# Kernel optimization log

Measured on AMD Instinct MI355X. Metric: run time of the kernel, lower is better.

The kernel has to match this reference:

```python
import jax, jax.numpy as jnp
import numpy as np

N = 50000
E = 800000
D_IN, D_HID, D_OUT = 128, 128, 64


def setup_inputs() -> dict:
    key = jax.random.key(0)
    ks = jax.random.split(key, 8)
    x = jax.random.normal(ks[0], (N, D_IN), dtype=jnp.float32)
    edge_index = jax.random.randint(ks[1], (2, E), 0, N, dtype=jnp.int64)
    # Glorot-ish init for GCNConv linear weights + zero bias (PyG default bias=True)
    def lin(k, din, dout):
        s = 1.0 / np.sqrt(din)
        return jax.random.uniform(k, (din, dout), jnp.float32, -s, s)
    return {
        "x": x,
        "edge_index": edge_index,
        "W1": lin(ks[2], D_IN, D_HID), "b1": jnp.zeros((D_HID,), jnp.float32),
        "W2": lin(ks[3], D_HID, D_HID), "b2": jnp.zeros((D_HID,), jnp.float32),
        "W3": lin(ks[4], D_HID, D_OUT), "b3": jnp.zeros((D_OUT,), jnp.float32),
    }


def _prep_edges(edge_index, n):
    # add self loops (PyG GCNConv default add_self_loops=True)
    loop = jnp.arange(n, dtype=edge_index.dtype)
    src = jnp.concatenate([edge_index[0], loop])
    dst = jnp.concatenate([edge_index[1], loop])
    deg = jax.ops.segment_sum(jnp.ones_like(dst, dtype=jnp.float32), dst, num_segments=n)
    dinv = jnp.where(deg > 0, jax.lax.rsqrt(deg), 0.0)
    norm = dinv[src] * dinv[dst]  # symmetric normalization per edge
    return src, dst, norm


def _gcn_conv(h, W, b, src, dst, norm, n):
    h = h @ W                                   # [N, dout]
    msg = h[src] * norm[:, None]                # [E+N, dout] gather
    out = jax.ops.segment_sum(msg, dst, num_segments=n)  # scatter-add
    return out + b


def reference(x, edge_index, W1, b1, W2, b2, W3, b3):
    src, dst, norm = _prep_edges(edge_index, N)
    h = jax.nn.relu(_gcn_conv(x, W1, b1, src, dst, norm, N))
    h = jax.nn.relu(_gcn_conv(h, W2, b2, src, dst, norm, N))
    return _gcn_conv(h, W3, b3, src, dst, norm, N)  # eval mode: dropout is identity
```

## Files before the change

kernel.cpp:

```cpp
#include <hip/hip_runtime.h>
#include <hip/hip_fp16.h>
#include <math.h>

#define NN 50000
#define NE 800000
#define RSTRIDE 104
#define RAWSTRIDE 96
#define NBUCK 196
#define BCAP 4608
#define ACH 4096

using bf8v = __attribute__((ext_vector_type(8))) short;
using f4v  = __attribute__((ext_vector_type(4))) float;

__device__ inline unsigned short f2bf(float f) {
    unsigned int u = __float_as_uint(f);
    u += 0x7FFFu + ((u >> 16) & 1u);
    return (unsigned short)(u >> 16);
}
__device__ inline float bflo(unsigned int d) { return __uint_as_float(d << 16); }
__device__ inline float bfhi(unsigned int d) { return __uint_as_float(d & 0xFFFF0000u); }
__device__ inline float ew(unsigned int u) {
    return __half2float(__ushort_as_half((unsigned short)(u >> 16)));
}
__device__ inline unsigned int epack(int col, float w) {
    return (unsigned int)col | ((unsigned int)__half_as_ushort(__float2half(w)) << 16);
}


__global__ __launch_bounds__(256) void bin_kernel(const int* __restrict__ src,
                                                  const int* __restrict__ dst,
                                                  int* __restrict__ gcursor,
                                                  unsigned int* __restrict__ bst) {
    __shared__ unsigned int items[ACH];
    __shared__ int cnt[256], pref[257], gstart[256];
    const int t = threadIdx.x;
    cnt[t] = 0;
    __syncthreads();
    const int base = blockIdx.x * ACH;

    unsigned int my[16]; int myb[16], myr[16];
    #pragma unroll
    for (int i = 0; i < 16; ++i) {
        int e = base + i * 256 + t;
        my[i] = 0; myb[i] = -1; myr[i] = 0;
        if (e < NE) {
            int d = dst[e], s = src[e];
            my[i] = (unsigned int)s | ((unsigned int)d << 16);
            int b = d >> 8;
            myb[i] = b;
            myr[i] = atomicAdd(&cnt[b], 1);
        }
    }
    __syncthreads();
    if (t == 0) {
        int run = 0;
        for (int b = 0; b < 256; ++b) { pref[b] = run; run += cnt[b]; }
        pref[256] = run;
    }
    __syncthreads();
    if (cnt[t] > 0) gstart[t] = atomicAdd(&gcursor[t], cnt[t]);
    __syncthreads();
    #pragma unroll
    for (int i = 0; i < 16; ++i)
        if (myb[i] >= 0) items[pref[myb[i]] + myr[i]] = my[i];
    __syncthreads();
    const int total = pref[256];
    for (int i = t; i < total; i += 256) {
        int lo = 0, hi = 255;
        while (lo < hi) { int mid = (lo + hi + 1) >> 1; if (pref[mid] <= i) lo = mid; else hi = mid - 1; }
        int idx = gstart[lo] + (i - pref[lo]);
        if (idx < BCAP) bst[(size_t)lo * BCAP + idx] = items[i];
    }
}


__global__ __launch_bounds__(512) void sortb_kernel(const int* __restrict__ gcursor,
                                                    const unsigned int* __restrict__ bst,
                                                    int* __restrict__ cnt_g,
                                                    float* __restrict__ dinv,
                                                    unsigned short* __restrict__ raw) {
    __shared__ unsigned int items[BCAP];
    __shared__ int cnt[256], pref[257], cur[256];
    __shared__ unsigned short outl[BCAP];
    const int b = blockIdx.x;
    const int t = threadIdx.x;
    int n = gcursor[b];
    if (n > BCAP) n = BCAP;
    if (t < 256) { cnt[t] = 0; cur[t] = 0; }
    __syncthreads();
    for (int i = t; i < n; i += 512) {
        unsigned int u = bst[(size_t)b * BCAP + i];
        items[i] = u;
        atomicAdd(&cnt[(u >> 16) & 255], 1);
    }
    __syncthreads();
    if (t == 0) {
        int run = 0;
        for (int j = 0; j < 256; ++j) { pref[j] = run; run += cnt[j]; }
        pref[256] = run;
    }
    __syncthreads();
    for (int i = t; i < n; i += 512) {
        unsigned int u = items[i];
        int ln = (u >> 16) & 255;
        int r = atomicAdd(&cur[ln], 1);
        outl[pref[ln] + r] = (unsigned short)(u & 0xFFFFu);
    }
    __syncthreads();
    for (int i = t; i < n; i += 512) {
        int lo = 0, hi = 255;
        while (lo < hi) { int mid = (lo + hi + 1) >> 1; if (pref[mid] <= i) lo = mid; else hi = mid - 1; }
        int r = i - pref[lo];
        if (r < RAWSTRIDE) raw[(size_t)(b * 256 + lo) * RAWSTRIDE + r] = outl[i];
    }
    if (t < 256) {
        int node = b * 256 + t;
        if (node < NN) {
            int c = cnt[t];
            cnt_g[node] = c;
            dinv[node] = rsqrtf((float)(1 + c));
        }
    }
}

__global__ __launch_bounds__(256) void finalize_kernel(const int* __restrict__ cnt_g,
                                                       const unsigned short* __restrict__ raw,
                                                       const float* __restrict__ dinv,
                                                       unsigned int* __restrict__ eg,
                                                       int* __restrict__ degp) {
    int i = blockIdx.x * 256 + threadIdx.x;
    if (i >= NN) return;
    int c = cnt_g[i];
    if (c > RAWSTRIDE) c = RAWSTRIDE;
    int deg = 1 + c;
    float di = dinv[i];
    unsigned int* row = eg + (size_t)i * RSTRIDE;
    const unsigned short* rrow = raw + (size_t)i * RAWSTRIDE;
    row[0] = epack(i, di * di);
    int p = 1;
    for (int r = 0; r < c; ++r) {
        int col = rrow[r];
        row[p++] = epack(col, di * dinv[col]);
    }
    int dp = (deg + 7) & ~7;
    for (; p < dp; ++p) row[p] = 0u;
    degp[i] = dp;
}


template <bool A_FP32>
__global__ __launch_bounds__(256) void mfma_gemm_kernel(const void* __restrict__ Ain,
                                                        const float* __restrict__ W,
                                                        unsigned short* __restrict__ out) {
    __shared__ unsigned short Wt[128 * 136];
    __shared__ unsigned short Dt[64 * 136];
    const int t = threadIdx.x;
    const int row0 = blockIdx.x * 64;

    {
        int n = t & 127;
        int kbase = (t >> 7) * 4;
        for (int kk = kbase; kk < 128; kk += 8) {
            float w0 = W[(kk + 0) * 128 + n];
            float w1 = W[(kk + 1) * 128 + n];
            float w2 = W[(kk + 2) * 128 + n];
            float w3 = W[(kk + 3) * 128 + n];
            unsigned int p0 = (unsigned int)f2bf(w0) | ((unsigned int)f2bf(w1) << 16);
            unsigned int p1 = (unsigned int)f2bf(w2) | ((unsigned int)f2bf(w3) << 16);
            *(unsigned int*)&Wt[n * 136 + kk]     = p0;
            *(unsigned int*)&Wt[n * 136 + kk + 2] = p1;
        }
    }
    __syncthreads();

    const int wave = t >> 6;
    const int lane = t & 63;
    const int m16  = lane & 15;
    const int quad = lane >> 4;
    const int arow = row0 + wave * 16 + m16;
    const int arowc = (arow < NN) ? arow : 0;

    f4v acc[8];
    #pragma unroll
    for (int i = 0; i < 8; ++i) acc[i] = (f4v)(0.0f);

    #pragma unroll
    for (int k0 = 0; k0 < 128; k0 += 32) {
        bf8v afrag;
        if (A_FP32) {
            const float* A = (const float*)Ain;
            const float4* ap = (const float4*)(A + (size_t)arowc * 128 + k0 + quad * 8);
            float4 a0 = ap[0], a1 = ap[1];
            afrag[0] = (short)f2bf(a0.x); afrag[1] = (short)f2bf(a0.y);
            afrag[2] = (short)f2bf(a0.z); afrag[3] = (short)f2bf(a0.w);
            afrag[4] = (short)f2bf(a1.x); afrag[5] = (short)f2bf(a1.y);
            afrag[6] = (short)f2bf(a1.z); afrag[7] = (short)f2bf(a1.w);
        } else {
            const unsigned short* A = (const unsigned short*)Ain;
            afrag = *(const bf8v*)(A + (size_t)arowc * 128 + k0 + quad * 8);
        }
        #pragma unroll
        for (int nt = 0; nt < 8; ++nt) {
            bf8v bfrag = *(const bf8v*)&Wt[(nt * 16 + m16) * 136 + k0 + quad * 8];
            acc[nt] = __builtin_amdgcn_mfma_f32_16x16x32_bf16(afrag, bfrag, acc[nt], 0, 0, 0);
        }
    }

    #pragma unroll
    for (int nt = 0; nt < 8; ++nt) {
        #pragma unroll
        for (int r = 0; r < 4; ++r) {
            Dt[(wave * 16 + quad * 4 + r) * 136 + nt * 16 + m16] = f2bf(acc[nt][r]);
        }
    }
    __syncthreads();

    {
        int r = t >> 2;
        int c = t & 3;
        int gr = row0 + r;
        if (gr < NN) {
            const uint4* s = (const uint4*)&Dt[r * 136] + c * 4;
            uint4* d = (uint4*)(out + (size_t)gr * 128) + c * 4;
            d[0] = s[0]; d[1] = s[1]; d[2] = s[2]; d[3] = s[3];
        }
    }
}


template <bool RELU>
__global__ __launch_bounds__(256) void agg_bf16_kernel(const unsigned short* __restrict__ hin,
                                                       const unsigned int* __restrict__ eg,
                                                       const int* __restrict__ degp,
                                                       const float* __restrict__ bias,
                                                       unsigned short* __restrict__ outb) {
    const int t = threadIdx.x;
    const int group = t >> 4;
    const int lane  = t & 15;
    const int wid = blockIdx.x * 16 + group;
    if (wid >= NN) return;

    const int dp = degp[wid];
    const unsigned int* row = eg + (size_t)wid * RSTRIDE;
    const uint4* hv = (const uint4*)hin;

    float acc[8] = {0.f, 0.f, 0.f, 0.f, 0.f, 0.f, 0.f, 0.f};

    for (int e = 0; e < dp; e += 8) {
        uint4 q0 = ((const uint4*)(row + e))[0];
        uint4 q1 = ((const uint4*)(row + e))[1];
        uint4 g0 = hv[(size_t)(q0.x & 0xFFFFu) * 16 + lane];
        uint4 g1 = hv[(size_t)(q0.y & 0xFFFFu) * 16 + lane];
        uint4 g2 = hv[(size_t)(q0.z & 0xFFFFu) * 16 + lane];
        uint4 g3 = hv[(size_t)(q0.w & 0xFFFFu) * 16 + lane];
        uint4 g4 = hv[(size_t)(q1.x & 0xFFFFu) * 16 + lane];
        uint4 g5 = hv[(size_t)(q1.y & 0xFFFFu) * 16 + lane];
        uint4 g6 = hv[(size_t)(q1.z & 0xFFFFu) * 16 + lane];
        uint4 g7 = hv[(size_t)(q1.w & 0xFFFFu) * 16 + lane];
        float w0 = ew(q0.x), w1 = ew(q0.y), w2 = ew(q0.z), w3 = ew(q0.w);
        float w4 = ew(q1.x), w5 = ew(q1.y), w6 = ew(q1.z), w7 = ew(q1.w);
        #define ACCUM(G, W_) \
            acc[0] += W_ * bflo(G.x); acc[1] += W_ * bfhi(G.x); \
            acc[2] += W_ * bflo(G.y); acc[3] += W_ * bfhi(G.y); \
            acc[4] += W_ * bflo(G.z); acc[5] += W_ * bfhi(G.z); \
            acc[6] += W_ * bflo(G.w); acc[7] += W_ * bfhi(G.w);
        ACCUM(g0, w0) ACCUM(g1, w1) ACCUM(g2, w2) ACCUM(g3, w3)
        ACCUM(g4, w4) ACCUM(g5, w5) ACCUM(g6, w6) ACCUM(g7, w7)
        #undef ACCUM
    }

    const float4* bp = (const float4*)bias;
    float4 b0 = bp[lane * 2], b1 = bp[lane * 2 + 1];
    acc[0] += b0.x; acc[1] += b0.y; acc[2] += b0.z; acc[3] += b0.w;
    acc[4] += b1.x; acc[5] += b1.y; acc[6] += b1.z; acc[7] += b1.w;
    if (RELU) {
        #pragma unroll
        for (int j = 0; j < 8; ++j) acc[j] = fmaxf(acc[j], 0.f);
    }
    uint4 o;
    o.x = (unsigned int)f2bf(acc[0]) | ((unsigned int)f2bf(acc[1]) << 16);
    o.y = (unsigned int)f2bf(acc[2]) | ((unsigned int)f2bf(acc[3]) << 16);
    o.z = (unsigned int)f2bf(acc[4]) | ((unsigned int)f2bf(acc[5]) << 16);
    o.w = (unsigned int)f2bf(acc[6]) | ((unsigned int)f2bf(acc[7]) << 16);
    ((uint4*)(outb + (size_t)wid * 128))[lane] = o;
}


__global__ __launch_bounds__(256) void gemm3_kernel(const unsigned short* __restrict__ Ab,
                                                    const float* __restrict__ W,
                                                    unsigned short* __restrict__ outh) {
    constexpr int CG = 16;
    constexpr int RPT = 4;
    constexpr int ROWS = 64;
    constexpr int LD = 132;
    __shared__ float lds[ROWS * LD];
    const int t = threadIdx.x;
    const int row0 = blockIdx.x * ROWS;

    #pragma unroll
    for (int j = 0; j < ROWS / 8; ++j) {
        int idx4 = j * 256 + t;
        int r = idx4 >> 5, c4 = idx4 & 31;
        int gr = row0 + r;
        uint2 u = make_uint2(0u, 0u);
        if (gr < NN) u = ((const uint2*)(Ab + (size_t)gr * 128))[c4];
        float4 v;
        v.x = bflo(u.x); v.y = bfhi(u.x); v.z = bflo(u.y); v.w = bfhi(u.y);
        ((float4*)(lds + r * LD))[c4] = v;
    }
    __syncthreads();

    const int cg = t % CG;
    const int rt = t / CG;
    const float4* Wv = (const float4*)W;
    float4 acc[RPT];
    #pragma unroll
    for (int i = 0; i < RPT; ++i) acc[i] = make_float4(0.f, 0.f, 0.f, 0.f);

    for (int k0 = 0; k0 < 128; k0 += 4) {
        float4 w0 = Wv[(k0 + 0) * CG + cg];
        float4 w1 = Wv[(k0 + 1) * CG + cg];
        float4 w2 = Wv[(k0 + 2) * CG + cg];
        float4 w3 = Wv[(k0 + 3) * CG + cg];
        #pragma unroll
        for (int i = 0; i < RPT; ++i) {
            const float* lr = lds + (rt * RPT + i) * LD;
            float4 a = ((const float4*)lr)[k0 >> 2];
            acc[i].x += a.x * w0.x + a.y * w1.x + a.z * w2.x + a.w * w3.x;
            acc[i].y += a.x * w0.y + a.y * w1.y + a.z * w2.y + a.w * w3.y;
            acc[i].z += a.x * w0.z + a.y * w1.z + a.z * w2.z + a.w * w3.z;
            acc[i].w += a.x * w0.w + a.y * w1.w + a.z * w2.w + a.w * w3.w;
        }
    }

    #pragma unroll
    for (int i = 0; i < RPT; ++i) {
        int gr = row0 + rt * RPT + i;
        if (gr < NN) {
            uint2 o;
            o.x = (unsigned int)f2bf(acc[i].x) | ((unsigned int)f2bf(acc[i].y) << 16);
            o.y = (unsigned int)f2bf(acc[i].z) | ((unsigned int)f2bf(acc[i].w) << 16);
            ((uint2*)(outh + (size_t)gr * 64))[cg] = o;
        }
    }
}


__global__ __launch_bounds__(256) void agg3_kernel(const unsigned short* __restrict__ hin,
                                                   const unsigned int* __restrict__ eg,
                                                   const int* __restrict__ degp,
                                                   const float* __restrict__ bias,
                                                   float* __restrict__ out) {
    const int t = threadIdx.x;
    const int group = t >> 3;
    const int lane  = t & 7;
    const int wid = blockIdx.x * 32 + group;
    if (wid >= NN) return;

    const int dp = degp[wid];
    const unsigned int* row = eg + (size_t)wid * RSTRIDE;
    const uint4* hv = (const uint4*)hin;

    float acc[8] = {0.f, 0.f, 0.f, 0.f, 0.f, 0.f, 0.f, 0.f};

    for (int e = 0; e < dp; e += 8) {
        uint4 q0 = ((const uint4*)(row + e))[0];
        uint4 q1 = ((const uint4*)(row + e))[1];
        uint4 g0 = hv[(size_t)(q0.x & 0xFFFFu) * 8 + lane];
        uint4 g1 = hv[(size_t)(q0.y & 0xFFFFu) * 8 + lane];
        uint4 g2 = hv[(size_t)(q0.z & 0xFFFFu) * 8 + lane];
        uint4 g3 = hv[(size_t)(q0.w & 0xFFFFu) * 8 + lane];
        uint4 g4 = hv[(size_t)(q1.x & 0xFFFFu) * 8 + lane];
        uint4 g5 = hv[(size_t)(q1.y & 0xFFFFu) * 8 + lane];
        uint4 g6 = hv[(size_t)(q1.z & 0xFFFFu) * 8 + lane];
        uint4 g7 = hv[(size_t)(q1.w & 0xFFFFu) * 8 + lane];
        float w0 = ew(q0.x), w1 = ew(q0.y), w2 = ew(q0.z), w3 = ew(q0.w);
        float w4 = ew(q1.x), w5 = ew(q1.y), w6 = ew(q1.z), w7 = ew(q1.w);
        #define ACCUM(G, W_) \
            acc[0] += W_ * bflo(G.x); acc[1] += W_ * bfhi(G.x); \
            acc[2] += W_ * bflo(G.y); acc[3] += W_ * bfhi(G.y); \
            acc[4] += W_ * bflo(G.z); acc[5] += W_ * bfhi(G.z); \
            acc[6] += W_ * bflo(G.w); acc[7] += W_ * bfhi(G.w);
        ACCUM(g0, w0) ACCUM(g1, w1) ACCUM(g2, w2) ACCUM(g3, w3)
        ACCUM(g4, w4) ACCUM(g5, w5) ACCUM(g6, w6) ACCUM(g7, w7)
        #undef ACCUM
    }

    const float4* bp = (const float4*)bias;
    float4 b0 = bp[lane * 2], b1 = bp[lane * 2 + 1];
    acc[0] += b0.x; acc[1] += b0.y; acc[2] += b0.z; acc[3] += b0.w;
    acc[4] += b1.x; acc[5] += b1.y; acc[6] += b1.z; acc[7] += b1.w;

    float4 o0 = make_float4(acc[0], acc[1], acc[2], acc[3]);
    float4 o1 = make_float4(acc[4], acc[5], acc[6], acc[7]);
    ((float4*)(out + (size_t)wid * 64))[lane * 2]     = o0;
    ((float4*)(out + (size_t)wid * 64))[lane * 2 + 1] = o1;
}


extern "C" void kernel_launch(void* const* d_in, const int* in_sizes, int n_in,
                              void* d_out, int out_size, void* d_ws, size_t ws_size,
                              hipStream_t stream) {
    const float* x  = (const float*)d_in[0];
    const int*   ei = (const int*)d_in[1];
    const float* W1 = (const float*)d_in[2];
    const float* b1 = (const float*)d_in[3];
    const float* W2 = (const float*)d_in[4];
    const float* b2 = (const float*)d_in[5];
    const float* W3 = (const float*)d_in[6];
    const float* b3 = (const float*)d_in[7];
    float* out = (float*)d_out;

    char* w = (char*)d_ws;
    int*   cnt_g   = (int*)  (w + 0x0000000);
    int*   gcursor = (int*)  (w + 0x0040000);
    float* dinv    = (float*)(w + 0x0048000);
    int*   degp    = (int*)  (w + 0x0080000);
    unsigned int*   eg  = (unsigned int*)  (w + 0x0140000);
    unsigned int*   bst = (unsigned int*)  (w + 0x1540000);
    unsigned short* hb  = (unsigned short*)(w + 0x1A00000);
    unsigned short* zb  = (unsigned short*)(w + 0x2680000);
    unsigned short* raw = (unsigned short*)(w + 0x2680000);
    unsigned short* h3b = (unsigned short*)(w + 0x3300000);

    const int* src = ei;
    const int* dst = ei + NE;

    hipMemsetAsync(gcursor, 0, NBUCK * sizeof(int), stream);
    bin_kernel<<<(NE + ACH - 1) / ACH, 256, 0, stream>>>(src, dst, gcursor, bst);
    sortb_kernel<<<NBUCK, 512, 0, stream>>>(gcursor, bst, cnt_g, dinv, raw);
    finalize_kernel<<<(NN + 255) / 256, 256, 0, stream>>>(cnt_g, raw, dinv, eg, degp);

    mfma_gemm_kernel<true><<<(NN + 63) / 64, 256, 0, stream>>>(x, W1, hb);
    agg_bf16_kernel<true><<<(NN + 15) / 16, 256, 0, stream>>>(hb, eg, degp, b1, zb);
    mfma_gemm_kernel<false><<<(NN + 63) / 64, 256, 0, stream>>>(zb, W2, hb);
    agg_bf16_kernel<true><<<(NN + 15) / 16, 256, 0, stream>>>(hb, eg, degp, b2, zb);
    gemm3_kernel<<<(NN + 63) / 64, 256, 0, stream>>>(zb, W3, h3b);
    agg3_kernel<<<(NN + 31) / 32, 256, 0, stream>>>(h3b, eg, degp, b3, out);
}
```

Baseline: 265.7 us.

## Merge edge binning with first GEMM and drop finalize pass in aggregation

Removes the finalize kernel that packed (col, fp16 weight) edge rows. The aggregation kernels now read the raw 16-bit neighbor lists and compute normalization weights on the fly from dinv, with the self-loop handled separately and a masked tail for partial groups of 8. Edge binning and the first GEMM are fused into one launch with block-index dispatch, so they can overlap and one launch is saved. In exchange, every aggregation pass does extra dinv gathers, and the fused kernel uses a larger shared allocation for all blocks, which may lower occupancy for the binning blocks.

```diff
diff --git a/kernel.cpp b/kernel.cpp
--- a/kernel.cpp
+++ b/kernel.cpp
@@ -4,11 +4,12 @@
 
 #define NN 50000
 #define NE 800000
-#define RSTRIDE 104
 #define RAWSTRIDE 96
 #define NBUCK 196
+#define NBBIN 196
 #define BCAP 4608
 #define ACH 4096
+#define G1B 782
 
 using bf8v = __attribute__((ext_vector_type(8))) short;
 using f4v  = __attribute__((ext_vector_type(4))) float;
@@ -20,24 +21,21 @@
 }
 __device__ inline float bflo(unsigned int d) { return __uint_as_float(d << 16); }
 __device__ inline float bfhi(unsigned int d) { return __uint_as_float(d & 0xFFFF0000u); }
-__device__ inline float ew(unsigned int u) {
-    return __half2float(__ushort_as_half((unsigned short)(u >> 16)));
-}
-__device__ inline unsigned int epack(int col, float w) {
-    return (unsigned int)col | ((unsigned int)__half_as_ushort(__float2half(w)) << 16);
-}
-
-
-__global__ __launch_bounds__(256) void bin_kernel(const int* __restrict__ src,
-                                                  const int* __restrict__ dst,
-                                                  int* __restrict__ gcursor,
-                                                  unsigned int* __restrict__ bst) {
-    __shared__ unsigned int items[ACH];
-    __shared__ int cnt[256], pref[257], gstart[256];
+
+
+__device__ __forceinline__ void bin_body(const int* __restrict__ src,
+                                         const int* __restrict__ dst,
+                                         int* __restrict__ gcursor,
+                                         unsigned int* __restrict__ bst,
+                                         int bx, char* shc) {
+    unsigned int* items = (unsigned int*)shc;
+    int* cnt    = (int*)(shc + 16384);
+    int* pref   = (int*)(shc + 17408);
+    int* gstart = (int*)(shc + 18436);
     const int t = threadIdx.x;
     cnt[t] = 0;
     __syncthreads();
-    const int base = blockIdx.x * ACH;
+    const int base = bx * ACH;
 
     unsigned int my[16]; int myb[16], myr[16];
     #pragma unroll
@@ -124,39 +122,16 @@
     }
 }
 
-__global__ __launch_bounds__(256) void finalize_kernel(const int* __restrict__ cnt_g,
-                                                       const unsigned short* __restrict__ raw,
-                                                       const float* __restrict__ dinv,
-                                                       unsigned int* __restrict__ eg,
-                                                       int* __restrict__ degp) {
-    int i = blockIdx.x * 256 + threadIdx.x;
-    if (i >= NN) return;
-    int c = cnt_g[i];
-    if (c > RAWSTRIDE) c = RAWSTRIDE;
-    int deg = 1 + c;
-    float di = dinv[i];
-    unsigned int* row = eg + (size_t)i * RSTRIDE;
-    const unsigned short* rrow = raw + (size_t)i * RAWSTRIDE;
-    row[0] = epack(i, di * di);
-    int p = 1;
-    for (int r = 0; r < c; ++r) {
-        int col = rrow[r];
-        row[p++] = epack(col, di * dinv[col]);
-    }
-    int dp = (deg + 7) & ~7;
-    for (; p < dp; ++p) row[p] = 0u;
-    degp[i] = dp;
-}
-
 
 template <bool A_FP32>
-__global__ __launch_bounds__(256) void mfma_gemm_kernel(const void* __restrict__ Ain,
-                                                        const float* __restrict__ W,
-                                                        unsigned short* __restrict__ out) {
-    __shared__ unsigned short Wt[128 * 136];
-    __shared__ unsigned short Dt[64 * 136];
+__device__ __forceinline__ void gemm128_body(const void* __restrict__ Ain,
+                                             const float* __restrict__ W,
+                                             unsigned short* __restrict__ out,
+                                             int bx, char* shc) {
+    unsigned short* Wt = (unsigned short*)shc;
+    unsigned short* Dt = (unsigned short*)(shc + 128 * 136 * 2);
     const int t = threadIdx.x;
-    const int row0 = blockIdx.x * 64;
+    const int row0 = bx * 64;
 
     {
         int n = t & 127;
@@ -228,11 +203,34 @@
     }
 }
 
+__global__ __launch_bounds__(256) void bin_g1_kernel(const int* __restrict__ src,
+                                                     const int* __restrict__ dst,
+                                                     int* __restrict__ gcursor,
+                                                     unsigned int* __restrict__ bst,
+                                                     const float* __restrict__ x,
+                                                     const float* __restrict__ W1,
+                                                     unsigned short* __restrict__ hb) {
+    __shared__ __align__(16) char sh[52224];
+    if (blockIdx.x < NBBIN) {
+        bin_body(src, dst, gcursor, bst, blockIdx.x, sh);
+    } else {
+        gemm128_body<true>(x, W1, hb, blockIdx.x - NBBIN, sh);
+    }
+}
+
+__global__ __launch_bounds__(256) void mfma_gemm_kernel(const unsigned short* __restrict__ Ain,
+                                                        const float* __restrict__ W,
+                                                        unsigned short* __restrict__ out) {
+    __shared__ __align__(16) char sh[52224];
+    gemm128_body<false>(Ain, W, out, blockIdx.x, sh);
+}
+
 
 template <bool RELU>
 __global__ __launch_bounds__(256) void agg_bf16_kernel(const unsigned short* __restrict__ hin,
-                                                       const unsigned int* __restrict__ eg,
-                                                       const int* __restrict__ degp,
+                                                       const unsigned short* __restrict__ raw,
+                                                       const int* __restrict__ cnt_g,
+                                                       const float* __restrict__ dinv,
                                                        const float* __restrict__ bias,
                                                        unsigned short* __restrict__ outb) {
     const int t = threadIdx.x;
@@ -241,34 +239,80 @@
     const int wid = blockIdx.x * 16 + group;
     if (wid >= NN) return;
 
-    const int dp = degp[wid];
-    const unsigned int* row = eg + (size_t)wid * RSTRIDE;
+    int c = cnt_g[wid];
+    if (c > RAWSTRIDE) c = RAWSTRIDE;
+    const float diw = dinv[wid];
+    const unsigned short* rrow = raw + (size_t)wid * RAWSTRIDE;
     const uint4* hv = (const uint4*)hin;
 
-    float acc[8] = {0.f, 0.f, 0.f, 0.f, 0.f, 0.f, 0.f, 0.f};
-
-    for (int e = 0; e < dp; e += 8) {
-        uint4 q0 = ((const uint4*)(row + e))[0];
-        uint4 q1 = ((const uint4*)(row + e))[1];
-        uint4 g0 = hv[(size_t)(q0.x & 0xFFFFu) * 16 + lane];
-        uint4 g1 = hv[(size_t)(q0.y & 0xFFFFu) * 16 + lane];
-        uint4 g2 = hv[(size_t)(q0.z & 0xFFFFu) * 16 + lane];
-        uint4 g3 = hv[(size_t)(q0.w & 0xFFFFu) * 16 + lane];
-        uint4 g4 = hv[(size_t)(q1.x & 0xFFFFu) * 16 + lane];
-        uint4 g5 = hv[(size_t)(q1.y & 0xFFFFu) * 16 + lane];
-        uint4 g6 = hv[(size_t)(q1.z & 0xFFFFu) * 16 + lane];
-        uint4 g7 = hv[(size_t)(q1.w & 0xFFFFu) * 16 + lane];
-        float w0 = ew(q0.x), w1 = ew(q0.y), w2 = ew(q0.z), w3 = ew(q0.w);
-        float w4 = ew(q1.x), w5 = ew(q1.y), w6 = ew(q1.z), w7 = ew(q1.w);
-        #define ACCUM(G, W_) \
-            acc[0] += W_ * bflo(G.x); acc[1] += W_ * bfhi(G.x); \
-            acc[2] += W_ * bflo(G.y); acc[3] += W_ * bfhi(G.y); \
-            acc[4] += W_ * bflo(G.z); acc[5] += W_ * bfhi(G.z); \
-            acc[6] += W_ * bflo(G.w); acc[7] += W_ * bfhi(G.w);
+    float acc[8];
+    {
+        uint4 g = hv[(size_t)wid * 16 + lane];
+        float ws = diw * diw;
+        acc[0] = ws * bflo(g.x); acc[1] = ws * bfhi(g.x);
+        acc[2] = ws * bflo(g.y); acc[3] = ws * bfhi(g.y);
+        acc[4] = ws * bflo(g.z); acc[5] = ws * bfhi(g.z);
+        acc[6] = ws * bflo(g.w); acc[7] = ws * bfhi(g.w);
+    }
+
+    #define ACCUM(G, W_) \
+        acc[0] += W_ * bflo(G.x); acc[1] += W_ * bfhi(G.x); \
+        acc[2] += W_ * bflo(G.y); acc[3] += W_ * bfhi(G.y); \
+        acc[4] += W_ * bflo(G.z); acc[5] += W_ * bfhi(G.z); \
+        acc[6] += W_ * bflo(G.w); acc[7] += W_ * bfhi(G.w);
+
+    const int cfull = c & ~7;
+    for (int e = 0; e < cfull; e += 8) {
+        uint4 q = *(const uint4*)(rrow + e);
+        int c0 = q.x & 0xFFFFu, c1 = q.x >> 16;
+        int c2 = q.y & 0xFFFFu, c3 = q.y >> 16;
+        int c4 = q.z & 0xFFFFu, c5 = q.z >> 16;
+        int c6 = q.w & 0xFFFFu, c7 = q.w >> 16;
+        float w0 = diw * dinv[c0], w1 = diw * dinv[c1];
+        float w2 = diw * dinv[c2], w3 = diw * dinv[c3];
+        float w4 = diw * dinv[c4], w5 = diw * dinv[c5];
+        float w6 = diw * dinv[c6], w7 = diw * dinv[c7];
+        uint4 g0 = hv[(size_t)c0 * 16 + lane];
+        uint4 g1 = hv[(size_t)c1 * 16 + lane];
+        uint4 g2 = hv[(size_t)c2 * 16 + lane];
+        uint4 g3 = hv[(size_t)c3 * 16 + lane];
+        uint4 g4 = hv[(size_t)c4 * 16 + lane];
+        uint4 g5 = hv[(size_t)c5 * 16 + lane];
+        uint4 g6 = hv[(size_t)c6 * 16 + lane];
+        uint4 g7 = hv[(size_t)c7 * 16 + lane];
         ACCUM(g0, w0) ACCUM(g1, w1) ACCUM(g2, w2) ACCUM(g3, w3)
         ACCUM(g4, w4) ACCUM(g5, w5) ACCUM(g6, w6) ACCUM(g7, w7)
-        #undef ACCUM
-    }
+    }
+    if (c & 7) {
+        int e = cfull, rem = c - e;
+        uint4 q = *(const uint4*)(rrow + e);
+        int c0 = q.x & 0xFFFFu, c1 = q.x >> 16;
+        int c2 = q.y & 0xFFFFu, c3 = q.y >> 16;
+        int c4 = q.z & 0xFFFFu, c5 = q.z >> 16;
+        int c6 = q.w & 0xFFFFu, c7 = q.w >> 16;
+        if (rem <= 1) c1 = 0; if (rem <= 2) c2 = 0; if (rem <= 3) c3 = 0;
+        if (rem <= 4) c4 = 0; if (rem <= 5) c5 = 0; if (rem <= 6) c6 = 0;
+        c7 = (rem <= 7) ? 0 : c7;
+        float w0 = diw * dinv[c0];
+        float w1 = (rem > 1) ? diw * dinv[c1] : 0.f;
+        float w2 = (rem > 2) ? diw * dinv[c2] : 0.f;
+        float w3 = (rem > 3) ? diw * dinv[c3] : 0.f;
+        float w4 = (rem > 4) ? diw * dinv[c4] : 0.f;
+        float w5 = (rem > 5) ? diw * dinv[c5] : 0.f;
+        float w6 = (rem > 6) ? diw * dinv[c6] : 0.f;
+        float w7 = 0.f;
+        uint4 g0 = hv[(size_t)c0 * 16 + lane];
+        uint4 g1 = hv[(size_t)c1 * 16 + lane];
+        uint4 g2 = hv[(size_t)c2 * 16 + lane];
+        uint4 g3 = hv[(size_t)c3 * 16 + lane];
+        uint4 g4 = hv[(size_t)c4 * 16 + lane];
+        uint4 g5 = hv[(size_t)c5 * 16 + lane];
+        uint4 g6 = hv[(size_t)c6 * 16 + lane];
+        uint4 g7 = hv[(size_t)c7 * 16 + lane];
+        ACCUM(g0, w0) ACCUM(g1, w1) ACCUM(g2, w2) ACCUM(g3, w3)
+        ACCUM(g4, w4) ACCUM(g5, w5) ACCUM(g6, w6) ACCUM(g7, w7)
+    }
+    #undef ACCUM
 
     const float4* bp = (const float4*)bias;
     float4 b0 = bp[lane * 2], b1 = bp[lane * 2 + 1];
@@ -348,8 +392,9 @@
 
 
 __global__ __launch_bounds__(256) void agg3_kernel(const unsigned short* __restrict__ hin,
-                                                   const unsigned int* __restrict__ eg,
-                                                   const int* __restrict__ degp,
+                                                   const unsigned short* __restrict__ raw,
+                                                   const int* __restrict__ cnt_g,
+                                                   const float* __restrict__ dinv,
                                                    const float* __restrict__ bias,
                                                    float* __restrict__ out) {
     const int t = threadIdx.x;
@@ -358,34 +403,80 @@
     const int wid = blockIdx.x * 32 + group;
     if (wid >= NN) return;
 
-    const int dp = degp[wid];
-    const unsigned int* row = eg + (size_t)wid * RSTRIDE;
+    int c = cnt_g[wid];
+    if (c > RAWSTRIDE) c = RAWSTRIDE;
+    const float diw = dinv[wid];
+    const unsigned short* rrow = raw + (size_t)wid * RAWSTRIDE;
     const uint4* hv = (const uint4*)hin;
 
-    float acc[8] = {0.f, 0.f, 0.f, 0.f, 0.f, 0.f, 0.f, 0.f};
-
-    for (int e = 0; e < dp; e += 8) {
-        uint4 q0 = ((const uint4*)(row + e))[0];
-        uint4 q1 = ((const uint4*)(row + e))[1];
-        uint4 g0 = hv[(size_t)(q0.x & 0xFFFFu) * 8 + lane];
-        uint4 g1 = hv[(size_t)(q0.y & 0xFFFFu) * 8 + lane];
-        uint4 g2 = hv[(size_t)(q0.z & 0xFFFFu) * 8 + lane];
-        uint4 g3 = hv[(size_t)(q0.w & 0xFFFFu) * 8 + lane];
-        uint4 g4 = hv[(size_t)(q1.x & 0xFFFFu) * 8 + lane];
-        uint4 g5 = hv[(size_t)(q1.y & 0xFFFFu) * 8 + lane];
-        uint4 g6 = hv[(size_t)(q1.z & 0xFFFFu) * 8 + lane];
-        uint4 g7 = hv[(size_t)(q1.w & 0xFFFFu) * 8 + lane];
-        float w0 = ew(q0.x), w1 = ew(q0.y), w2 = ew(q0.z), w3 = ew(q0.w);
-        float w4 = ew(q1.x), w5 = ew(q1.y), w6 = ew(q1.z), w7 = ew(q1.w);
-        #define ACCUM(G, W_) \
-            acc[0] += W_ * bflo(G.x); acc[1] += W_ * bfhi(G.x); \
-            acc[2] += W_ * bflo(G.y); acc[3] += W_ * bfhi(G.y); \
-            acc[4] += W_ * bflo(G.z); acc[5] += W_ * bfhi(G.z); \
-            acc[6] += W_ * bflo(G.w); acc[7] += W_ * bfhi(G.w);
+    float acc[8];
+    {
+        uint4 g = hv[(size_t)wid * 8 + lane];
+        float ws = diw * diw;
+        acc[0] = ws * bflo(g.x); acc[1] = ws * bfhi(g.x);
+        acc[2] = ws * bflo(g.y); acc[3] = ws * bfhi(g.y);
+        acc[4] = ws * bflo(g.z); acc[5] = ws * bfhi(g.z);
+        acc[6] = ws * bflo(g.w); acc[7] = ws * bfhi(g.w);
+    }
+
+    #define ACCUM(G, W_) \
+        acc[0] += W_ * bflo(G.x); acc[1] += W_ * bfhi(G.x); \
+        acc[2] += W_ * bflo(G.y); acc[3] += W_ * bfhi(G.y); \
+        acc[4] += W_ * bflo(G.z); acc[5] += W_ * bfhi(G.z); \
+        acc[6] += W_ * bflo(G.w); acc[7] += W_ * bfhi(G.w);
+
+    const int cfull = c & ~7;
+    for (int e = 0; e < cfull; e += 8) {
+        uint4 q = *(const uint4*)(rrow + e);
+        int c0 = q.x & 0xFFFFu, c1 = q.x >> 16;
+        int c2 = q.y & 0xFFFFu, c3 = q.y >> 16;
+        int c4 = q.z & 0xFFFFu, c5 = q.z >> 16;
+        int c6 = q.w & 0xFFFFu, c7 = q.w >> 16;
+        float w0 = diw * dinv[c0], w1 = diw * dinv[c1];
+        float w2 = diw * dinv[c2], w3 = diw * dinv[c3];
+        float w4 = diw * dinv[c4], w5 = diw * dinv[c5];
+        float w6 = diw * dinv[c6], w7 = diw * dinv[c7];
+        uint4 g0 = hv[(size_t)c0 * 8 + lane];
+        uint4 g1 = hv[(size_t)c1 * 8 + lane];
+        uint4 g2 = hv[(size_t)c2 * 8 + lane];
+        uint4 g3 = hv[(size_t)c3 * 8 + lane];
+        uint4 g4 = hv[(size_t)c4 * 8 + lane];
+        uint4 g5 = hv[(size_t)c5 * 8 + lane];
+        uint4 g6 = hv[(size_t)c6 * 8 + lane];
+        uint4 g7 = hv[(size_t)c7 * 8 + lane];
         ACCUM(g0, w0) ACCUM(g1, w1) ACCUM(g2, w2) ACCUM(g3, w3)
         ACCUM(g4, w4) ACCUM(g5, w5) ACCUM(g6, w6) ACCUM(g7, w7)
-        #undef ACCUM
-    }
+    }
+    if (c & 7) {
+        int e = cfull, rem = c - e;
+        uint4 q = *(const uint4*)(rrow + e);
+        int c0 = q.x & 0xFFFFu, c1 = q.x >> 16;
+        int c2 = q.y & 0xFFFFu, c3 = q.y >> 16;
+        int c4 = q.z & 0xFFFFu, c5 = q.z >> 16;
+        int c6 = q.w & 0xFFFFu, c7 = q.w >> 16;
+        if (rem <= 1) c1 = 0; if (rem <= 2) c2 = 0; if (rem <= 3) c3 = 0;
+        if (rem <= 4) c4 = 0; if (rem <= 5) c5 = 0; if (rem <= 6) c6 = 0;
+        c7 = (rem <= 7) ? 0 : c7;
+        float w0 = diw * dinv[c0];
+        float w1 = (rem > 1) ? diw * dinv[c1] : 0.f;
+        float w2 = (rem > 2) ? diw * dinv[c2] : 0.f;
+        float w3 = (rem > 3) ? diw * dinv[c3] : 0.f;
+        float w4 = (rem > 4) ? diw * dinv[c4] : 0.f;
+        float w5 = (rem > 5) ? diw * dinv[c5] : 0.f;
+        float w6 = (rem > 6) ? diw * dinv[c6] : 0.f;
+        float w7 = 0.f;
+        uint4 g0 = hv[(size_t)c0 * 8 + lane];
+        uint4 g1 = hv[(size_t)c1 * 8 + lane];
+        uint4 g2 = hv[(size_t)c2 * 8 + lane];
+        uint4 g3 = hv[(size_t)c3 * 8 + lane];
+        uint4 g4 = hv[(size_t)c4 * 8 + lane];
+        uint4 g5 = hv[(size_t)c5 * 8 + lane];
+        uint4 g6 = hv[(size_t)c6 * 8 + lane];
+        uint4 g7 = hv[(size_t)c7 * 8 + lane];
+        ACCUM(g0, w0) ACCUM(g1, w1) ACCUM(g2, w2) ACCUM(g3, w3)
+        ACCUM(g4, w4) ACCUM(g5, w5) ACCUM(g6, w6) ACCUM(g7, w7)
+    }
+    #undef ACCUM
 
     const float4* bp = (const float4*)bias;
     float4 b0 = bp[lane * 2], b1 = bp[lane * 2 + 1];
@@ -416,26 +507,21 @@
     int*   cnt_g   = (int*)  (w + 0x0000000);
     int*   gcursor = (int*)  (w + 0x0040000);
     float* dinv    = (float*)(w + 0x0048000);
-    int*   degp    = (int*)  (w + 0x0080000);
-    unsigned int*   eg  = (unsigned int*)  (w + 0x0140000);
-    unsigned int*   bst = (unsigned int*)  (w + 0x1540000);
-    unsigned short* hb  = (unsigned short*)(w + 0x1A00000);
-    unsigned short* zb  = (unsigned short*)(w + 0x2680000);
-    unsigned short* raw = (unsigned short*)(w + 0x2680000);
-    unsigned short* h3b = (unsigned short*)(w + 0x3300000);
+    unsigned int*   bst = (unsigned int*)  (w + 0x0080000);
+    unsigned short* raw = (unsigned short*)(w + 0x0400000);
+    unsigned short* hb  = (unsigned short*)(w + 0x0E00000);
+    unsigned short* zb  = (unsigned short*)(w + 0x1B00000);
+    unsigned short* h3b = (unsigned short*)(w + 0x2800000);
 
     const int* src = ei;
     const int* dst = ei + NE;
 
     hipMemsetAsync(gcursor, 0, NBUCK * sizeof(int), stream);
-    bin_kernel<<<(NE + ACH - 1) / ACH, 256, 0, stream>>>(src, dst, gcursor, bst);
+    bin_g1_kernel<<<NBBIN + G1B, 256, 0, stream>>>(src, dst, gcursor, bst, x, W1, hb);
     sortb_kernel<<<NBUCK, 512, 0, stream>>>(gcursor, bst, cnt_g, dinv, raw);
-    finalize_kernel<<<(NN + 255) / 256, 256, 0, stream>>>(cnt_g, raw, dinv, eg, degp);
-
-    mfma_gemm_kernel<true><<<(NN + 63) / 64, 256, 0, stream>>>(x, W1, hb);
-    agg_bf16_kernel<true><<<(NN + 15) / 16, 256, 0, stream>>>(hb, eg, degp, b1, zb);
-    mfma_gemm_kernel<false><<<(NN + 63) / 64, 256, 0, stream>>>(zb, W2, hb);
-    agg_bf16_kernel<true><<<(NN + 15) / 16, 256, 0, stream>>>(hb, eg, degp, b2, zb);
-    gemm3_kernel<<<(NN + 63) / 64, 256, 0, stream>>>(zb, W3, h3b);
-    agg3_kernel<<<(NN + 31) / 32, 256, 0, stream>>>(h3b, eg, degp, b3, out);
-}
+    agg_bf16_kernel<true><<<(NN + 15) / 16, 256, 0, stream>>>(hb, raw, cnt_g, dinv, b1, zb);
+    mfma_gemm_kernel<<<G1B, 256, 0, stream>>>(zb, W2, hb);
+    agg_bf16_kernel<true><<<(NN + 15) / 16, 256, 0, stream>>>(hb, raw, cnt_g, dinv, b2, zb);
+    gemm3_kernel<<<G1B, 256, 0, stream>>>(zb, W3, h3b);
+    agg3_kernel<<<(NN + 31) / 32, 256, 0, stream>>>(h3b, raw, cnt_g, dinv, b3, out);
+}
```

New measurement: 244.8 us. 7.9% less time.
